# Kernel tuning notes

Measured on AMD Instinct MI355X. Metric: run time of the kernel, lower is better.

## Reference

```python
import jax, jax.numpy as jnp
import numpy as np

N_FREQS = 8
ALPHA = 16.0
SCALING = ALPHA / N_FREQS  # alpha / n_freqs
EPS = 1e-8


def setup_inputs() -> dict:
    key = jax.random.key(0)
    ks = jax.random.split(key, 6)
    B, S, IN, OUT = 4, 2048, 4096, 4096
    x = jax.random.normal(ks[0], (B, S, IN), dtype=jnp.float32)
    W = jax.random.normal(ks[1], (OUT, IN), dtype=jnp.float32) * 0.02
    bias = jax.random.normal(ks[2], (OUT,), dtype=jnp.float32) * 0.02
    delta_real = jax.random.normal(ks[3], (N_FREQS, N_FREQS), dtype=jnp.float32)
    delta_imag = jax.random.normal(ks[4], (N_FREQS, N_FREQS), dtype=jnp.float32)
    # m is initialized in torch as row-norm of the base weight; emulate that here
    m = jnp.linalg.norm(W, axis=1, keepdims=True)
    return {"x": x, "W": W, "bias": bias,
            "delta_real": delta_real, "delta_imag": delta_imag, "m": m}


def _dora_weight(W, delta_real, delta_imag, m):
    # full-size rfft2 of the frozen base weight (norm='ortho')
    W_fft = jnp.fft.rfft2(W, norm="ortho")            # [OUT, IN//2+1] complex
    fh, fw = delta_real.shape                          # freq_h, freq_w (low-freq corner)
    delta = jax.lax.complex(delta_real, delta_imag) * SCALING
    W_fft = W_fft.at[:fh, :fw].add(delta)              # pad-to-full + add, fused
    W_mod = jnp.fft.irfft2(W_fft, s=W.shape, norm="ortho")  # [OUT, IN] real
    # DoRA: magnitude m times unit row-direction
    norm = jnp.linalg.norm(W_mod, axis=1, keepdims=True)     # [OUT, 1]
    return m * W_mod / (norm + EPS)


def reference(x, W, bias, delta_real, delta_imag, m):
    W_dora = _dora_weight(W, delta_real, delta_imag, m)      # [OUT, IN]
    # F.linear: x @ W^T + b
    return jnp.einsum("bsi,oi->bso", x, W_dora) + bias
```

## Files before the change

kernel.cpp:

```cpp
#include <hip/hip_runtime.h>
#include <hip/hip_bf16.h>

typedef __attribute__((ext_vector_type(4))) float f32x4;
typedef __attribute__((ext_vector_type(8))) short bf16x8;

#define IN_DIM 4096
#define OUT_DIM 4096
#define MROWS 8192
#define NFREQ 8
#define TWO_PI 6.283185307179586f

#define BK 64
#define NT (IN_DIM / BK)
#define LDS_BUF 32768
#define LDS_HALF 16384
#define LDS_B_REGION 65536

__device__ __forceinline__ unsigned int f2bf(float f) {
    union { float f; unsigned int u; } a;
    a.f = f;
    unsigned int u = a.u;
    u += 0x7fffu + ((u >> 16) & 1u);
    return u >> 16;
}

#define ROT_C 0.9999988234517019f
#define ROT_S 0.0015339801862847655f

__global__ __launch_bounds__(256) void prep_kernel(
    const float* __restrict__ x,
    const float* __restrict__ W,
    const float* __restrict__ dre,
    const float* __restrict__ dimg,
    const float* __restrict__ mrow,
    unsigned short* __restrict__ Wd,
    unsigned short* __restrict__ xb)
{
    const int t = threadIdx.x;

    if (blockIdx.x >= OUT_DIM) {
        const size_t idx = (size_t)(blockIdx.x - OUT_DIM) * 256 + t;
        const f32x4* p = (const f32x4*)(x + idx * 8);
        const f32x4 a = p[0], b = p[1];
        uint4 o;
        o.x = f2bf(a[0]) | (f2bf(a[1]) << 16);
        o.y = f2bf(a[2]) | (f2bf(a[3]) << 16);
        o.z = f2bf(b[0]) | (f2bf(b[1]) << 16);
        o.w = f2bf(b[2]) | (f2bf(b[3]) << 16);
        *(uint4*)(xb + idx * 8) = o;
        return;
    }

    const int o = blockIdx.x;

    float P[NFREQ], Q[NFREQ];
#pragma unroll
    for (int w = 0; w < NFREQ; ++w) { P[w] = 0.f; Q[w] = 0.f; }
#pragma unroll
    for (int h = 0; h < NFREQ; ++h) {
        const float th = (TWO_PI / 4096.0f) * (float)((h * o) & 4095);
        const float sh = __sinf(th), ch = __cosf(th);
#pragma unroll
        for (int w = 0; w < NFREQ; ++w) {
            const float A = 2.0f * dre[h * NFREQ + w];
            const float B = 2.0f * dimg[h * NFREQ + w];
            P[w] += A * ch - B * sh;
            Q[w] += A * sh + B * ch;
        }
    }
#pragma unroll
    for (int w = 0; w < NFREQ; ++w) {
        const float c = (w == 0 ? 1.0f : 2.0f) * (1.0f / 4096.0f);
        P[w] *= c; Q[w] *= c;
    }

    const int i0 = t * 16;
    const f32x4* wrow = (const f32x4*)(W + (size_t)o * IN_DIM + i0);
    float vals[16];
    float ss = 0.0f;

    const float beta0 = (TWO_PI / 4096.0f) * (float)i0;
    float cb = __cosf(beta0), sb = __sinf(beta0);

#pragma unroll
    for (int q = 0; q < 4; ++q) {
        const f32x4 wv = wrow[q];
#pragma unroll
        for (int j = 0; j < 4; ++j) {
            float cw = cb, sw = sb;
            float d = P[0] + P[1] * cw - Q[1] * sw;
#pragma unroll
            for (int w = 2; w < NFREQ; ++w) {
                const float cn = cw * cb - sw * sb;
                sw = sw * cb + cw * sb;
                cw = cn;
                d += P[w] * cw - Q[w] * sw;
            }
            const float v = wv[j] + d;
            vals[q * 4 + j] = v;
            ss += v * v;
            const float cbn = cb * ROT_C - sb * ROT_S;
            sb = sb * ROT_C + cb * ROT_S;
            cb = cbn;
        }
    }

#pragma unroll
    for (int off = 32; off > 0; off >>= 1)
        ss += __shfl_down(ss, off, 64);
    __shared__ float red[4];
    if ((t & 63) == 0) red[t >> 6] = ss;
    __syncthreads();
    const float n2 = red[0] + red[1] + red[2] + red[3];
    const float scale = mrow[o] / (sqrtf(n2) + 1e-8f);

    unsigned int wds[8];
#pragma unroll
    for (int k = 0; k < 8; ++k)
        wds[k] = f2bf(vals[2 * k] * scale) | (f2bf(vals[2 * k + 1] * scale) << 16);
    uint4* dst = (uint4*)(Wd + (size_t)o * IN_DIM + i0);
    dst[0] = make_uint4(wds[0], wds[1], wds[2], wds[3]);
    dst[1] = make_uint4(wds[4], wds[5], wds[6], wds[7]);
}


#define GLOAD(src, ldsoff)                                                    \
    __builtin_amdgcn_global_load_lds(                                         \
        (const __attribute__((address_space(1))) void*)(src),                 \
        (__attribute__((address_space(3))) void*)(smem + (ldsoff)), 16, 0, 0)

#define SBAR      asm volatile("s_barrier" ::: "memory")
#define WAITLGKM0 asm volatile("s_waitcnt lgkmcnt(0)" ::: "memory")

__global__ __launch_bounds__(256, 1) void gemm8_kernel(
    const unsigned short* __restrict__ Xb,
    const unsigned short* __restrict__ Wd,
    const float* __restrict__ bias,
    float* __restrict__ out)
{
    __shared__ __align__(1024) unsigned char smem[131072];

    const int tid = threadIdx.x;
    const int wid = tid >> 6, lane = tid & 63;
    const int wr = wid >> 1, wc = wid & 1;
    const int fr = lane & 15, fq = lane >> 4;

    const int bid = blockIdx.x;
    const int xcd = bid & 7;
    const int u = bid >> 3;
    const int tm = u >> 1;
    const int tn = 2 * xcd + (u & 1);
    const int m0 = tm * 256, n0 = tn * 256;

    const int srr = wid * 32 + (lane >> 3);
    const int scc = ((lane & 7) ^ ((lane >> 3) & 7)) * 8;
    const unsigned short* aS = Xb + (size_t)(m0 + srr) * IN_DIM + scc;
    const unsigned short* bS = Wd + (size_t)(n0 + srr) * IN_DIM + scc;
    const int sdst = wid * 4096;

    const int cbyte = ((fq ^ (fr & 7)) * 16);
    const int aBase0 = (wr * 128 + fr) * 128 + cbyte;
    const int aBase1 = aBase0 ^ 64;
    const int bBase0 = LDS_B_REGION + (wc * 128 + fr) * 128 + cbyte;
    const int bBase1 = bBase0 ^ 64;

    auto STAGE = [&](int buf, int isB, int half, int tt) {
        const unsigned short* s =
            (isB ? bS : aS) + (size_t)half * 128 * IN_DIM + (size_t)tt * BK;
        const int d = buf * LDS_BUF + isB * LDS_B_REGION + half * LDS_HALF + sdst;
#pragma unroll
        for (int j = 0; j < 4; ++j)
            GLOAD(s + (size_t)j * 8 * IN_DIM, d + j * 1024);
    };

    f32x4 acc[8][8] = {};
    bf16x8 a0[4][2], a1[4][2], bb[4][2];

    STAGE(0, 0, 0, 0); STAGE(0, 0, 1, 0);
    STAGE(0, 1, 0, 0); STAGE(0, 1, 1, 0);
    STAGE(1, 0, 0, 1); STAGE(1, 0, 1, 1);
    STAGE(1, 1, 0, 1);
    asm volatile("s_waitcnt vmcnt(12)" ::: "memory");
    SBAR;

    for (int t = 0; t < NT; ++t) {
        const int b = t & 1;
        const int bo = b * LDS_BUF;
        const bool st1 = (t + 1 < NT);
        const bool st2 = (t + 2 < NT);

#pragma unroll
        for (int mf = 0; mf < 4; ++mf) {
            a0[mf][0] = *(const bf16x8*)(smem + bo + aBase0 + mf * 2048);
            a0[mf][1] = *(const bf16x8*)(smem + bo + aBase1 + mf * 2048);
        }
#pragma unroll
        for (int nf = 0; nf < 4; ++nf) {
            bb[nf][0] = *(const bf16x8*)(smem + bo + bBase0 + nf * 2048);
            bb[nf][1] = *(const bf16x8*)(smem + bo + bBase1 + nf * 2048);
        }
        if (st1) STAGE(b ^ 1, 1, 1, t + 1);
        __builtin_amdgcn_s_setprio(1);
#pragma unroll
        for (int ks = 0; ks < 2; ++ks)
#pragma unroll
            for (int mf = 0; mf < 4; ++mf)
#pragma unroll
                for (int nf = 0; nf < 4; ++nf)
                    acc[mf][nf] = __builtin_amdgcn_mfma_f32_16x16x32_bf16(
                        a0[mf][ks], bb[nf][ks], acc[mf][nf], 0, 0, 0);
        __builtin_amdgcn_s_setprio(0);

#pragma unroll
        for (int mf = 0; mf < 4; ++mf) {
            a1[mf][0] = *(const bf16x8*)(smem + bo + aBase0 + 8192 + mf * 2048);
            a1[mf][1] = *(const bf16x8*)(smem + bo + aBase1 + 8192 + mf * 2048);
        }
        __builtin_amdgcn_s_setprio(1);
#pragma unroll
        for (int ks = 0; ks < 2; ++ks)
#pragma unroll
            for (int mf = 0; mf < 4; ++mf)
#pragma unroll
                for (int nf = 0; nf < 4; ++nf)
                    acc[4 + mf][nf] = __builtin_amdgcn_mfma_f32_16x16x32_bf16(
                        a1[mf][ks], bb[nf][ks], acc[4 + mf][nf], 0, 0, 0);
        __builtin_amdgcn_s_setprio(0);
        WAITLGKM0;
        SBAR;

#pragma unroll
        for (int nf = 0; nf < 4; ++nf) {
            bb[nf][0] = *(const bf16x8*)(smem + bo + bBase0 + 8192 + nf * 2048);
            bb[nf][1] = *(const bf16x8*)(smem + bo + bBase1 + 8192 + nf * 2048);
        }
        if (st2) STAGE(b, 0, 0, t + 2);
        __builtin_amdgcn_s_setprio(1);
#pragma unroll
        for (int ks = 0; ks < 2; ++ks)
#pragma unroll
            for (int mf = 0; mf < 4; ++mf)
#pragma unroll
                for (int nf = 0; nf < 4; ++nf)
                    acc[4 + mf][4 + nf] = __builtin_amdgcn_mfma_f32_16x16x32_bf16(
                        a1[mf][ks], bb[nf][ks], acc[4 + mf][4 + nf], 0, 0, 0);
        __builtin_amdgcn_s_setprio(0);
        WAITLGKM0;
        SBAR;

        if (st2) { STAGE(b, 0, 1, t + 2); STAGE(b, 1, 0, t + 2); }
        __builtin_amdgcn_s_setprio(1);
#pragma unroll
        for (int ks = 0; ks < 2; ++ks)
#pragma unroll
            for (int mf = 0; mf < 4; ++mf)
#pragma unroll
                for (int nf = 0; nf < 4; ++nf)
                    acc[mf][4 + nf] = __builtin_amdgcn_mfma_f32_16x16x32_bf16(
                        a0[mf][ks], bb[nf][ks], acc[mf][4 + nf], 0, 0, 0);
        __builtin_amdgcn_s_setprio(0);
        if (st2) {
            asm volatile("s_waitcnt vmcnt(12)" ::: "memory");
        } else {
            asm volatile("s_waitcnt vmcnt(0)" ::: "memory");
        }
        SBAR;
    }

#pragma unroll
    for (int nf = 0; nf < 8; ++nf) {
        const int col = n0 + wc * 128 + nf * 16 + fr;
        const float bv = bias[col];
#pragma unroll
        for (int mf = 0; mf < 8; ++mf) {
            const int row = m0 + wr * 128 + mf * 16 + fq * 4;
            float* op = out + (size_t)row * OUT_DIM + col;
            op[0 * OUT_DIM] = acc[mf][nf][0] + bv;
            op[1 * OUT_DIM] = acc[mf][nf][1] + bv;
            op[2 * OUT_DIM] = acc[mf][nf][2] + bv;
            op[3 * OUT_DIM] = acc[mf][nf][3] + bv;
        }
    }
}

__global__ __launch_bounds__(256) void gemm_fallback(
    const float* __restrict__ Xf,
    const unsigned short* __restrict__ Wd,
    const float* __restrict__ bias,
    float* __restrict__ out)
{
    __shared__ unsigned short As[2][128 * 32];
    __shared__ unsigned short Bs[2][128 * 32];

    const int t = threadIdx.x;
    const int wid = t >> 6, lane = t & 63;
    const int wr = wid >> 1, wc = wid & 1;
    const int m0 = blockIdx.x * 128, n0 = blockIdx.y * 128;
    const int fr = lane & 15, fq = lane >> 4;

    f32x4 acc[4][4] = {};

    const int srow = wid * 16 + (lane >> 2);
    const int scol = (lane & 3) * 8;
    const unsigned short* bsrc0 = Wd + (size_t)(n0 + srow) * IN_DIM + scol;
    const unsigned short* bsrc1 = bsrc0 + (size_t)64 * IN_DIM;
    const int lds_off = wid * 512;

    const int ar = t >> 1;
    const int ak = (t & 1) * 16;
    const float* afp = Xf + (size_t)(m0 + ar) * IN_DIM + ak;
    const int a_lds_off = ar * 32 + ak;

    auto stageB = [&](unsigned short* ldsbase, int kt) {
        __builtin_amdgcn_global_load_lds(
            (const __attribute__((address_space(1))) void*)(bsrc0 + kt * 32),
            (__attribute__((address_space(3))) void*)(ldsbase + lds_off), 16, 0, 0);
        __builtin_amdgcn_global_load_lds(
            (const __attribute__((address_space(1))) void*)(bsrc1 + kt * 32),
            (__attribute__((address_space(3))) void*)(ldsbase + 2048 + lds_off), 16, 0, 0);
    };
    auto writeA = [&](int buf, const f32x4* v) {
        unsigned int w[8];
#pragma unroll
        for (int k = 0; k < 4; ++k) {
            w[2 * k]     = f2bf(v[k][0]) | (f2bf(v[k][1]) << 16);
            w[2 * k + 1] = f2bf(v[k][2]) | (f2bf(v[k][3]) << 16);
        }
        uint4* d = (uint4*)(&As[buf][a_lds_off]);
        d[0] = make_uint4(w[0], w[1], w[2], w[3]);
        d[1] = make_uint4(w[4], w[5], w[6], w[7]);
    };

    stageB(Bs[0], 0);
    {
        f32x4 av[4];
        const f32x4* ap = (const f32x4*)afp;
        av[0] = ap[0]; av[1] = ap[1]; av[2] = ap[2]; av[3] = ap[3];
        writeA(0, av);
    }
    __syncthreads();

    for (int kt = 0; kt < IN_DIM / 32; ++kt) {
        const int cur = kt & 1;
        const bool more = (kt + 1 < IN_DIM / 32);
        f32x4 nv[4];
        if (more) {
            const f32x4* ap = (const f32x4*)(afp + (size_t)(kt + 1) * 32);
            nv[0] = ap[0]; nv[1] = ap[1]; nv[2] = ap[2]; nv[3] = ap[3];
            stageB(Bs[cur ^ 1], kt + 1);
        }
        bf16x8 afrag[4], bfrag[4];
#pragma unroll
        for (int mf = 0; mf < 4; ++mf)
            afrag[mf] = *(const bf16x8*)(&As[cur][(wr * 64 + mf * 16 + fr) * 32 + fq * 8]);
#pragma unroll
        for (int nf = 0; nf < 4; ++nf)
            bfrag[nf] = *(const bf16x8*)(&Bs[cur][(wc * 64 + nf * 16 + fr) * 32 + fq * 8]);
#pragma unroll
        for (int mf = 0; mf < 4; ++mf)
#pragma unroll
            for (int nf = 0; nf < 4; ++nf)
                acc[mf][nf] = __builtin_amdgcn_mfma_f32_16x16x32_bf16(
                    afrag[mf], bfrag[nf], acc[mf][nf], 0, 0, 0);
        if (more) writeA(cur ^ 1, nv);
        __syncthreads();
    }

#pragma unroll
    for (int nf = 0; nf < 4; ++nf) {
        const int col = n0 + wc * 64 + nf * 16 + fr;
        const float bv = bias[col];
#pragma unroll
        for (int mf = 0; mf < 4; ++mf) {
            const int row = m0 + wr * 64 + mf * 16 + fq * 4;
            float* op = out + (size_t)row * OUT_DIM + col;
            op[0 * OUT_DIM] = acc[mf][nf][0] + bv;
            op[1 * OUT_DIM] = acc[mf][nf][1] + bv;
            op[2 * OUT_DIM] = acc[mf][nf][2] + bv;
            op[3 * OUT_DIM] = acc[mf][nf][3] + bv;
        }
    }
}

extern "C" void kernel_launch(void* const* d_in, const int* in_sizes, int n_in,
                              void* d_out, int out_size, void* d_ws, size_t ws_size,
                              hipStream_t stream) {
    const float* x    = (const float*)d_in[0];
    const float* W    = (const float*)d_in[1];
    const float* bias = (const float*)d_in[2];
    const float* dre  = (const float*)d_in[3];
    const float* dimg = (const float*)d_in[4];
    const float* mrow = (const float*)d_in[5];
    float* out = (float*)d_out;

    unsigned short* Wd = (unsigned short*)d_ws;
    const size_t WD_BYTES = (size_t)OUT_DIM * IN_DIM * 2;
    const size_t XB_BYTES = (size_t)MROWS * IN_DIM * 2;
    unsigned short* Xb = (unsigned short*)((char*)d_ws + WD_BYTES);
    const bool fast = ws_size >= WD_BYTES + XB_BYTES;

    if (fast) {
        const int cvt_blocks = (MROWS * (size_t)IN_DIM / 8) / 256;
        prep_kernel<<<OUT_DIM + cvt_blocks, 256, 0, stream>>>(
            x, W, dre, dimg, mrow, Wd, Xb);
        gemm8_kernel<<<dim3((MROWS / 256) * (OUT_DIM / 256)), dim3(256), 0, stream>>>(
            Xb, Wd, bias, out);
    } else {
        prep_kernel<<<OUT_DIM, 256, 0, stream>>>(x, W, dre, dimg, mrow, Wd, Wd);
        dim3 grid(MROWS / 128, OUT_DIM / 128);
        gemm_fallback<<<grid, dim3(256), 0, stream>>>(x, Wd, bias, out);
    }
}
```

Before: 354.7 us.

## Shrink GEMM tile to 128x256 with K=32 steps for two blocks per CU

Replaces the 256x256 tile, BK=64 bf16 GEMM with a 128x256 tile stepping K by 32, using 48KB LDS and launch bounds that allow two workgroups per CU. The grid doubles and each wave holds a 64x128 accumulator instead of 128x128. The aim is higher occupancy and better latency hiding, at the cost of lower arithmetic intensity per tile, more global traffic for the reused W operand, and twice as many barrier iterations.

```diff
diff --git a/kernel.cpp b/kernel.cpp
--- a/kernel.cpp
+++ b/kernel.cpp
@@ -9,12 +9,6 @@
 #define MROWS 8192
 #define NFREQ 8
 #define TWO_PI 6.283185307179586f
-
-#define BK 64
-#define NT (IN_DIM / BK)
-#define LDS_BUF 32768
-#define LDS_HALF 16384
-#define LDS_B_REGION 65536
 
 __device__ __forceinline__ unsigned int f2bf(float f) {
     union { float f; unsigned int u; } a;
@@ -132,13 +126,13 @@
 #define SBAR      asm volatile("s_barrier" ::: "memory")
 #define WAITLGKM0 asm volatile("s_waitcnt lgkmcnt(0)" ::: "memory")
 
-__global__ __launch_bounds__(256, 1) void gemm8_kernel(
+__global__ __launch_bounds__(256, 2) void gemm_k32_kernel(
     const unsigned short* __restrict__ Xb,
     const unsigned short* __restrict__ Wd,
     const float* __restrict__ bias,
     float* __restrict__ out)
 {
-    __shared__ __align__(1024) unsigned char smem[131072];
+    __shared__ __align__(1024) unsigned char smem[49152];
 
     const int tid = threadIdx.x;
     const int wid = tid >> 6, lane = tid & 63;
@@ -150,117 +144,77 @@
     const int u = bid >> 3;
     const int tm = u >> 1;
     const int tn = 2 * xcd + (u & 1);
-    const int m0 = tm * 256, n0 = tn * 256;
-
-    const int srr = wid * 32 + (lane >> 3);
-    const int scc = ((lane & 7) ^ ((lane >> 3) & 7)) * 8;
-    const unsigned short* aS = Xb + (size_t)(m0 + srr) * IN_DIM + scc;
-    const unsigned short* bS = Wd + (size_t)(n0 + srr) * IN_DIM + scc;
-    const int sdst = wid * 4096;
-
-    const int cbyte = ((fq ^ (fr & 7)) * 16);
-    const int aBase0 = (wr * 128 + fr) * 128 + cbyte;
-    const int aBase1 = aBase0 ^ 64;
-    const int bBase0 = LDS_B_REGION + (wc * 128 + fr) * 128 + cbyte;
-    const int bBase1 = bBase0 ^ 64;
-
-    auto STAGE = [&](int buf, int isB, int half, int tt) {
-        const unsigned short* s =
-            (isB ? bS : aS) + (size_t)half * 128 * IN_DIM + (size_t)tt * BK;
-        const int d = buf * LDS_BUF + isB * LDS_B_REGION + half * LDS_HALF + sdst;
-#pragma unroll
-        for (int j = 0; j < 4; ++j)
-            GLOAD(s + (size_t)j * 8 * IN_DIM, d + j * 1024);
+    const int m0 = tm * 128, n0 = tn * 256;
+
+    const int srow = wid * 16 + (lane >> 2);
+    const int scc = ((lane & 3) ^ ((lane >> 2) & 3)) * 8;
+    const unsigned short* aS = Xb + (size_t)(m0 + srow) * IN_DIM + scc;
+    const unsigned short* bS = Wd + (size_t)(n0 + srow) * IN_DIM + scc;
+    const int sdst = wid * 1024;
+
+    const int cb4 = ((fq ^ (fr & 3)) * 16);
+    const int aB = (wr * 64 + fr) * 64 + cb4;
+    const int bB = (wc * 128 + fr) * 64 + cb4;
+
+    auto STAGEA = [&](int buf, int tt) {
+#pragma unroll
+        for (int g = 0; g < 2; ++g)
+            GLOAD(aS + (size_t)(g * 64) * IN_DIM + (size_t)tt * 32,
+                  buf * 8192 + g * 4096 + sdst);
     };
-
-    f32x4 acc[8][8] = {};
-    bf16x8 a0[4][2], a1[4][2], bb[4][2];
-
-    STAGE(0, 0, 0, 0); STAGE(0, 0, 1, 0);
-    STAGE(0, 1, 0, 0); STAGE(0, 1, 1, 0);
-    STAGE(1, 0, 0, 1); STAGE(1, 0, 1, 1);
-    STAGE(1, 1, 0, 1);
-    asm volatile("s_waitcnt vmcnt(12)" ::: "memory");
+    auto STAGEB = [&](int buf, int tt) {
+#pragma unroll
+        for (int g = 0; g < 4; ++g)
+            GLOAD(bS + (size_t)(g * 64) * IN_DIM + (size_t)tt * 32,
+                  16384 + buf * 16384 + g * 4096 + sdst);
+    };
+
+    f32x4 acc[4][8] = {};
+    bf16x8 af[4], bf[8];
+
+    STAGEA(0, 0);
+    STAGEB(0, 0);
+    STAGEA(1, 1);
+    asm volatile("s_waitcnt vmcnt(2)" ::: "memory");
     SBAR;
 
-    for (int t = 0; t < NT; ++t) {
+    const int NT2 = IN_DIM / 32;
+    for (int t = 0; t < NT2; ++t) {
         const int b = t & 1;
-        const int bo = b * LDS_BUF;
-        const bool st1 = (t + 1 < NT);
-        const bool st2 = (t + 2 < NT);
-
-#pragma unroll
-        for (int mf = 0; mf < 4; ++mf) {
-            a0[mf][0] = *(const bf16x8*)(smem + bo + aBase0 + mf * 2048);
-            a0[mf][1] = *(const bf16x8*)(smem + bo + aBase1 + mf * 2048);
-        }
-#pragma unroll
-        for (int nf = 0; nf < 4; ++nf) {
-            bb[nf][0] = *(const bf16x8*)(smem + bo + bBase0 + nf * 2048);
-            bb[nf][1] = *(const bf16x8*)(smem + bo + bBase1 + nf * 2048);
-        }
-        if (st1) STAGE(b ^ 1, 1, 1, t + 1);
+        const int boA = b * 8192;
+        const int boB = 16384 + b * 16384;
+        const bool st1 = (t + 1 < NT2);
+        const bool st2 = (t + 2 < NT2);
+
+#pragma unroll
+        for (int mf = 0; mf < 4; ++mf)
+            af[mf] = *(const bf16x8*)(smem + boA + aB + mf * 1024);
+#pragma unroll
+        for (int nf = 0; nf < 8; ++nf)
+            bf[nf] = *(const bf16x8*)(smem + boB + bB + nf * 1024);
+        if (st1) STAGEB(b ^ 1, t + 1);
         __builtin_amdgcn_s_setprio(1);
 #pragma unroll
-        for (int ks = 0; ks < 2; ++ks)
-#pragma unroll
-            for (int mf = 0; mf < 4; ++mf)
-#pragma unroll
-                for (int nf = 0; nf < 4; ++nf)
-                    acc[mf][nf] = __builtin_amdgcn_mfma_f32_16x16x32_bf16(
-                        a0[mf][ks], bb[nf][ks], acc[mf][nf], 0, 0, 0);
-        __builtin_amdgcn_s_setprio(0);
-
-#pragma unroll
-        for (int mf = 0; mf < 4; ++mf) {
-            a1[mf][0] = *(const bf16x8*)(smem + bo + aBase0 + 8192 + mf * 2048);
-            a1[mf][1] = *(const bf16x8*)(smem + bo + aBase1 + 8192 + mf * 2048);
-        }
-        __builtin_amdgcn_s_setprio(1);
-#pragma unroll
-        for (int ks = 0; ks < 2; ++ks)
-#pragma unroll
-            for (int mf = 0; mf < 4; ++mf)
-#pragma unroll
-                for (int nf = 0; nf < 4; ++nf)
-                    acc[4 + mf][nf] = __builtin_amdgcn_mfma_f32_16x16x32_bf16(
-                        a1[mf][ks], bb[nf][ks], acc[4 + mf][nf], 0, 0, 0);
+        for (int mf = 0; mf < 4; ++mf)
+#pragma unroll
+            for (int nf = 0; nf < 4; ++nf)
+                acc[mf][nf] = __builtin_amdgcn_mfma_f32_16x16x32_bf16(
+                    af[mf], bf[nf], acc[mf][nf], 0, 0, 0);
         __builtin_amdgcn_s_setprio(0);
         WAITLGKM0;
         SBAR;
 
-#pragma unroll
-        for (int nf = 0; nf < 4; ++nf) {
-            bb[nf][0] = *(const bf16x8*)(smem + bo + bBase0 + 8192 + nf * 2048);
-            bb[nf][1] = *(const bf16x8*)(smem + bo + bBase1 + 8192 + nf * 2048);
-        }
-        if (st2) STAGE(b, 0, 0, t + 2);
+        if (st2) STAGEA(b, t + 2);
         __builtin_amdgcn_s_setprio(1);
 #pragma unroll
-        for (int ks = 0; ks < 2; ++ks)
-#pragma unroll
-            for (int mf = 0; mf < 4; ++mf)
-#pragma unroll
-                for (int nf = 0; nf < 4; ++nf)
-                    acc[4 + mf][4 + nf] = __builtin_amdgcn_mfma_f32_16x16x32_bf16(
-                        a1[mf][ks], bb[nf][ks], acc[4 + mf][4 + nf], 0, 0, 0);
-        __builtin_amdgcn_s_setprio(0);
-        WAITLGKM0;
-        SBAR;
-
-        if (st2) { STAGE(b, 0, 1, t + 2); STAGE(b, 1, 0, t + 2); }
-        __builtin_amdgcn_s_setprio(1);
-#pragma unroll
-        for (int ks = 0; ks < 2; ++ks)
-#pragma unroll
-            for (int mf = 0; mf < 4; ++mf)
-#pragma unroll
-                for (int nf = 0; nf < 4; ++nf)
-                    acc[mf][4 + nf] = __builtin_amdgcn_mfma_f32_16x16x32_bf16(
-                        a0[mf][ks], bb[nf][ks], acc[mf][4 + nf], 0, 0, 0);
+        for (int mf = 0; mf < 4; ++mf)
+#pragma unroll
+            for (int nf = 4; nf < 8; ++nf)
+                acc[mf][nf] = __builtin_amdgcn_mfma_f32_16x16x32_bf16(
+                    af[mf], bf[nf], acc[mf][nf], 0, 0, 0);
         __builtin_amdgcn_s_setprio(0);
         if (st2) {
-            asm volatile("s_waitcnt vmcnt(12)" ::: "memory");
+            asm volatile("s_waitcnt vmcnt(2)" ::: "memory");
         } else {
             asm volatile("s_waitcnt vmcnt(0)" ::: "memory");
         }
@@ -272,8 +226,8 @@
         const int col = n0 + wc * 128 + nf * 16 + fr;
         const float bv = bias[col];
 #pragma unroll
-        for (int mf = 0; mf < 8; ++mf) {
-            const int row = m0 + wr * 128 + mf * 16 + fq * 4;
+        for (int mf = 0; mf < 4; ++mf) {
+            const int row = m0 + wr * 64 + mf * 16 + fq * 4;
             float* op = out + (size_t)row * OUT_DIM + col;
             op[0 * OUT_DIM] = acc[mf][nf][0] + bv;
             op[1 * OUT_DIM] = acc[mf][nf][1] + bv;
@@ -403,7 +357,7 @@
         const int cvt_blocks = (MROWS * (size_t)IN_DIM / 8) / 256;
         prep_kernel<<<OUT_DIM + cvt_blocks, 256, 0, stream>>>(
             x, W, dre, dimg, mrow, Wd, Xb);
-        gemm8_kernel<<<dim3((MROWS / 256) * (OUT_DIM / 256)), dim3(256), 0, stream>>>(
+        gemm_k32_kernel<<<dim3((MROWS / 128) * (OUT_DIM / 256)), dim3(256), 0, stream>>>(
             Xb, Wd, bias, out);
     } else {
         prep_kernel<<<OUT_DIM, 256, 0, stream>>>(x, W, dre, dimg, mrow, Wd, Wd);
```

Measured after the change: 329.4 us. 7.1% less time.
